# Kernel optimization log

Hardware: AMD Instinct MI355X
Metric: run time of the kernel (lower is better)

The kernel has to match this reference:

```python
import jax, jax.numpy as jnp
import numpy as np
import math

INPUT_SIZE = 128  # feature dim D, from init_kwargs

def setup_inputs() -> dict:
    key = jax.random.key(0)
    k1, k2 = jax.random.split(key)
    B, N, D = 4, 4096, INPUT_SIZE
    inp = jax.random.normal(k1, (B, N, D), dtype=jnp.float32)
    adj = jax.random.randint(k2, (B, N, N), 0, 2, dtype=jnp.int32)
    return {"input": inp, "adj": adj}

def reference(input, adj):
    # scores: [B, N, N] = X X^T / sqrt(D)
    scores = jnp.matmul(input, jnp.swapaxes(input, 1, 2)) / math.sqrt(INPUT_SIZE)
    neg = jnp.asarray(-1e12, dtype=scores.dtype)
    masked = jnp.where(adj > 0, scores, neg)
    attention = jax.nn.softmax(masked, axis=2)
    out_hid = jnp.matmul(attention, input)  # [B, N, D]
    return out_hid
```

## Files before the change

kernel.cpp:

```cpp
#include <hip/hip_runtime.h>
#include <hip/hip_bf16.h>


#define NN 4096
#define DD 128
#define BK 128
#define NT (NN / BK)

#define XBT_REL 32768
#define BUF1_OFF 65536
#define P_OFF 131072
#define P_WSTRIDE 2304
#define LDS_BYTES (P_OFF + 8 * P_WSTRIDE)

typedef __attribute__((ext_vector_type(8))) short bf16x8;
typedef __attribute__((ext_vector_type(16))) float f32x16;

static __device__ __forceinline__ unsigned f2bf(float f) {
    union { float f; unsigned u; } v; v.f = f;
    return (v.u + 0x7fffu + ((v.u >> 16) & 1u)) >> 16;
}

static __device__ __forceinline__ void gl_lds16(const void* g, void* l) {
    __builtin_amdgcn_global_load_lds(
        (const __attribute__((address_space(1))) unsigned*)g,
        (__attribute__((address_space(3))) unsigned*)l, 16, 0, 0);
}

__global__ __launch_bounds__(256)
void gat_prep(const float* __restrict__ X, unsigned short* __restrict__ xb,
              unsigned short* __restrict__ xbt) {
    __shared__ unsigned short tile[64][132];
    const int t = threadIdx.x;
    const int b  = blockIdx.x >> 6;
    const int kc = blockIdx.x & 63;
    const float* src = X + ((size_t)b * NN + kc * 64) * DD;
    unsigned short* xbo = xb + ((size_t)b * NN + kc * 64) * DD;

    #pragma unroll
    for (int it = 0; it < 8; ++it) {
        int f = it * 256 + t;
        int k = f >> 5, d4 = (f & 31) * 4;
        float4 v = *(const float4*)(src + (size_t)f * 4);
        uint2 pk;
        pk.x = f2bf(v.x) | (f2bf(v.y) << 16);
        pk.y = f2bf(v.z) | (f2bf(v.w) << 16);
        *(uint2*)(xbo + (size_t)f * 4) = pk;
        *(uint2*)(&tile[k][d4]) = pk;
    }
    __syncthreads();
    const int d = t >> 1, kb0 = (t & 1) * 32;
    unsigned short* dst = xbt + (size_t)b * DD * NN + (size_t)d * NN + kc * 64 + kb0;
    #pragma unroll
    for (int c = 0; c < 4; ++c) {
        union { uint4 o; unsigned short e[8]; } u;
        #pragma unroll
        for (int j = 0; j < 8; ++j) u.e[j] = tile[kb0 + c * 8 + j][d];
        *(uint4*)(dst + c * 8) = u.o;
    }
}

__global__ __launch_bounds__(512, 2)
void gat_fused(const unsigned short* __restrict__ xb,
               const unsigned short* __restrict__ xbt,
               const int* __restrict__ adj,
               float* __restrict__ out) {
    extern __shared__ char lds[];
    const int t = threadIdx.x;
    const int w = t >> 6, l = t & 63;
    const int l32 = l & 31, h5 = l >> 5;
    const int rw = w >> 2;
    const int kh = w & 3;
    const int bid  = blockIdx.x;
    const int b    = bid >> 6;
    const int row0 = (bid & 63) * 64;
    const int qbase = row0 + rw * 32;
    const int kbase = kh * 32;

    const char* xb_b  = (const char*)(xb  + (size_t)b * NN * DD);
    const char* xbt_b = (const char*)(xbt + (size_t)b * DD * NN);
    const int*  Ag    = adj + (size_t)b * NN * NN;
    float*      Og    = out + (size_t)b * NN * DD;

    bf16x8 qfrag[8];
    {
        const char* qp = xb_b + (size_t)(qbase + l32) * 256;
        #pragma unroll
        for (int c = 0; c < 8; ++c)
            qfrag[c] = *(const bf16x8*)(qp + c * 32 + h5 * 16);
    }

    int off_xb[4], off_xbt[4];
    #pragma unroll
    for (int j = 0; j < 4; ++j) {
        int r = w * 16 + 4 * j + (l >> 4);
        off_xb[j]  = r * 256      + (((l & 15) ^ (r & 7)) * 16);
        off_xbt[j] = r * (NN * 2) + (((l & 15) ^ (r & 7)) * 16);
    }
    char* bufA = lds;
    char* bufB = lds + BUF1_OFF;
    char* pw   = lds + P_OFF + w * P_WSTRIDE;
    const int* arow = Ag + (size_t)(qbase + l32) * NN + kbase + 4 * h5;

#define STAGE(BUF, KEY0) do {                                                  \
    _Pragma("unroll")                                                          \
    for (int j = 0; j < 4; ++j) {                                              \
        gl_lds16(xb_b  + (size_t)(KEY0) * 256 + off_xb[j],                     \
                 (BUF) + w * 4096 + j * 1024);                                 \
        gl_lds16(xbt_b + (size_t)(KEY0) * 2 + off_xbt[j],                      \
                 (BUF) + XBT_REL + w * 4096 + j * 1024);                       \
    }                                                                          \
} while (0)

    STAGE(bufA, 0);
    int4 avA[4];
    #pragma unroll
    for (int g = 0; g < 4; ++g) avA[g] = *(const int4*)(arow + g * 8);

    f32x16 oacc[4];
    #pragma unroll
    for (int d = 0; d < 4; ++d) oacc[d] = (f32x16)(0.0f);
    float psum = 0.f;

#define COMPUTE(BUF, AV) do {                                                  \
    f32x16 sacc = (f32x16)(0.0f);                                              \
    {                                                                          \
        const int krow = kbase + l32;                                          \
        const char* kp = (BUF) + krow * 256;                                   \
        const int sw = krow & 7;                                               \
        _Pragma("unroll")                                                      \
        for (int c = 0; c < 8; ++c) {                                          \
            bf16x8 kf = *(const bf16x8*)(kp + (((2 * c + h5) ^ sw) * 16));     \
            sacc = __builtin_amdgcn_mfma_f32_32x32x16_bf16(                    \
                kf, qfrag[c], sacc, 0, 0, 0);                                  \
        }                                                                      \
    }                                                                          \
    {                                                                          \
        const float SC = 0.08838834764831845f;                \
        _Pragma("unroll")                                                      \
        for (int g = 0; g < 4; ++g) {                                          \
            int4 a = (AV)[g];                                                  \
            float p0 = (a.x > 0) ? __expf(sacc[4 * g + 0] * SC) : 0.f;         \
            float p1 = (a.y > 0) ? __expf(sacc[4 * g + 1] * SC) : 0.f;         \
            float p2 = (a.z > 0) ? __expf(sacc[4 * g + 2] * SC) : 0.f;         \
            float p3 = (a.w > 0) ? __expf(sacc[4 * g + 3] * SC) : 0.f;         \
            psum += p0 + p1 + p2 + p3;                                         \
            uint2 pk;                                                          \
            pk.x = f2bf(p0) | (f2bf(p1) << 16);                                \
            pk.y = f2bf(p2) | (f2bf(p3) << 16);                                \
            *(uint2*)(pw + l32 * 72 + g * 16 + h5 * 8) = pk;                   \
        }                                                                      \
    }                                                                          \
    {                                                                          \
        bf16x8 pf0 = *(const bf16x8*)(pw + l32 * 72 + h5 * 16);                \
        bf16x8 pf1 = *(const bf16x8*)(pw + l32 * 72 + 32 + h5 * 16);           \
        _Pragma("unroll")                                                      \
        for (int db = 0; db < 4; ++db) {                                       \
            const int vrow = db * 32 + l32;                                    \
            const int swv = vrow & 7;                                          \
            const char* vp = (BUF) + XBT_REL + vrow * 256;                     \
            bf16x8 v0 = *(const bf16x8*)(vp + (((4 * kh + h5) ^ swv) * 16));   \
            oacc[db] = __builtin_amdgcn_mfma_f32_32x32x16_bf16(                \
                pf0, v0, oacc[db], 0, 0, 0);                                   \
            bf16x8 v1 = *(const bf16x8*)(vp + (((4 * kh + 2 + h5) ^ swv) * 16)); \
            oacc[db] = __builtin_amdgcn_mfma_f32_32x32x16_bf16(                \
                pf1, v1, oacc[db], 0, 0, 0);                                   \
        }                                                                      \
    }                                                                          \
} while (0)

    for (int kt = 0; kt < NT - 1; ++kt) {
        int4 avB[4];
        #pragma unroll
        for (int g = 0; g < 4; ++g)
            avB[g] = *(const int4*)(arow + (kt + 1) * BK + g * 8);
        asm volatile("s_waitcnt vmcnt(4)" ::: "memory");
        __builtin_amdgcn_s_barrier();
        STAGE(bufB, (kt + 1) * BK);
        COMPUTE(bufA, avA);
        char* tmp = bufA; bufA = bufB; bufB = tmp;
        #pragma unroll
        for (int g = 0; g < 4; ++g) avA[g] = avB[g];
    }
    asm volatile("s_waitcnt vmcnt(0)" ::: "memory");
    __builtin_amdgcn_s_barrier();
    COMPUTE(bufA, avA);

    psum += __shfl_xor(psum, 32, 64);
    __syncthreads();

    float* slot = (float*)(lds + w * 17408);
    #pragma unroll
    for (int db = 0; db < 4; ++db)
        #pragma unroll
        for (int r = 0; r < 16; ++r) {
            const int lrow = (r & 3) + 8 * (r >> 2) + 4 * h5;
            slot[lrow * 136 + db * 32 + l32] = oacc[db][r];
        }
    float* psarea = (float*)(lds + 139264);
    if (l < 32) psarea[w * 32 + l] = psum;
    __syncthreads();

    {
        const int R   = w * 8 + (l >> 3);
        const int q32 = R & 31, rwR = R >> 5;
        const int d0  = (l & 7) * 16;
        float tot = psarea[(rwR * 4 + 0) * 32 + q32]
                  + psarea[(rwR * 4 + 1) * 32 + q32]
                  + psarea[(rwR * 4 + 2) * 32 + q32]
                  + psarea[(rwR * 4 + 3) * 32 + q32];
        float invt = 1.0f / tot;
        float4 acc[4];
        #pragma unroll
        for (int j = 0; j < 4; ++j) acc[j] = (float4){0.f, 0.f, 0.f, 0.f};
        #pragma unroll
        for (int kx = 0; kx < 4; ++kx) {
            const float* sp = (const float*)(lds + (rwR * 4 + kx) * 17408)
                              + q32 * 136 + d0;
            #pragma unroll
            for (int j = 0; j < 4; ++j) {
                float4 v = *(const float4*)(sp + 4 * j);
                acc[j].x += v.x; acc[j].y += v.y;
                acc[j].z += v.z; acc[j].w += v.w;
            }
        }
        float* op = Og + (size_t)(row0 + R) * DD + d0;
        #pragma unroll
        for (int j = 0; j < 4; ++j) {
            float4 res;
            res.x = acc[j].x * invt; res.y = acc[j].y * invt;
            res.z = acc[j].z * invt; res.w = acc[j].w * invt;
            *(float4*)(op + 4 * j) = res;
        }
    }
#undef COMPUTE
#undef STAGE
}

extern "C" void kernel_launch(void* const* d_in, const int* in_sizes, int n_in,
                              void* d_out, int out_size, void* d_ws, size_t ws_size,
                              hipStream_t stream) {
    const float* X   = (const float*)d_in[0];
    const int*   adj = (const int*)d_in[1];
    float*       out = (float*)d_out;
    unsigned short* xb  = (unsigned short*)d_ws;
    unsigned short* xbt = xb + (size_t)4 * NN * DD;

    hipFuncSetAttribute((const void*)gat_fused,
                        hipFuncAttributeMaxDynamicSharedMemorySize, LDS_BYTES);
    gat_prep<<<dim3(256), dim3(256), 0, stream>>>(X, xb, xbt);
    gat_fused<<<dim3(256), dim3(512), LDS_BYTES, stream>>>(xb, xbt, adj, out);
}
```

Before: 415.4 us.

## Repack softmax probabilities in registers via permlane swap; prefetch adjacency two tiles ahead

Drops the per-wave LDS round trip that re-laid the bf16 probability tile from accumulator layout into MFMA A-operand layout. It now packs pairs with v_cvt_pk_bf16_f32 and exchanges halves across the wave with v_permlane32_swap. It also deepens the adjacency-mask prefetch from one tile ahead to two, hiding more global latency on the dominant int32 stream, and shrinks LDS use. The cost is more live registers, and the s_waitcnt vmcnt(4) count may no longer fit the extra in-flight loads, which could stall the loop or break its ordering.

```diff
diff --git a/kernel.cpp b/kernel.cpp
--- a/kernel.cpp
+++ b/kernel.cpp
@@ -9,9 +9,8 @@
 
 #define XBT_REL 32768
 #define BUF1_OFF 65536
-#define P_OFF 131072
-#define P_WSTRIDE 2304
-#define LDS_BYTES (P_OFF + 8 * P_WSTRIDE)
+#define PS_OFF 139264
+#define LDS_BYTES (PS_OFF + 1024)
 
 typedef __attribute__((ext_vector_type(8))) short bf16x8;
 typedef __attribute__((ext_vector_type(16))) float f32x16;
@@ -25,6 +24,15 @@
     __builtin_amdgcn_global_load_lds(
         (const __attribute__((address_space(1))) unsigned*)g,
         (__attribute__((address_space(3))) unsigned*)l, 16, 0, 0);
+}
+
+static __device__ __forceinline__ unsigned cvtpk(float lo, float hi) {
+    unsigned r;
+    asm("v_cvt_pk_bf16_f32 %0, %1, %2" : "=v"(r) : "v"(lo), "v"(hi));
+    return r;
+}
+static __device__ __forceinline__ void plswap(unsigned& a, unsigned& b) {
+    asm volatile("v_permlane32_swap_b32 %0, %1" : "+v"(a), "+v"(b));
 }
 
 __global__ __launch_bounds__(256)
@@ -99,7 +107,6 @@
     }
     char* bufA = lds;
     char* bufB = lds + BUF1_OFF;
-    char* pw   = lds + P_OFF + w * P_WSTRIDE;
     const int* arow = Ag + (size_t)(qbase + l32) * NN + kbase + 4 * h5;
 
 #define STAGE(BUF, KEY0) do {                                                  \
@@ -113,9 +120,11 @@
 } while (0)
 
     STAGE(bufA, 0);
-    int4 avA[4];
+    int4 avA[4], avB[4], avC[4];
     #pragma unroll
     for (int g = 0; g < 4; ++g) avA[g] = *(const int4*)(arow + g * 8);
+    #pragma unroll
+    for (int g = 0; g < 4; ++g) avB[g] = *(const int4*)(arow + BK + g * 8);
 
     f32x16 oacc[4];
     #pragma unroll
@@ -135,25 +144,33 @@
                 kf, qfrag[c], sacc, 0, 0, 0);                                  \
         }                                                                      \
     }                                                                          \
+    float p[16];                                                               \
     {                                                                          \
         const float SC = 0.08838834764831845f;                \
         _Pragma("unroll")                                                      \
         for (int g = 0; g < 4; ++g) {                                          \
             int4 a = (AV)[g];                                                  \
-            float p0 = (a.x > 0) ? __expf(sacc[4 * g + 0] * SC) : 0.f;         \
-            float p1 = (a.y > 0) ? __expf(sacc[4 * g + 1] * SC) : 0.f;         \
-            float p2 = (a.z > 0) ? __expf(sacc[4 * g + 2] * SC) : 0.f;         \
-            float p3 = (a.w > 0) ? __expf(sacc[4 * g + 3] * SC) : 0.f;         \
-            psum += p0 + p1 + p2 + p3;                                         \
-            uint2 pk;                                                          \
-            pk.x = f2bf(p0) | (f2bf(p1) << 16);                                \
-            pk.y = f2bf(p2) | (f2bf(p3) << 16);                                \
-            *(uint2*)(pw + l32 * 72 + g * 16 + h5 * 8) = pk;                   \
+            p[4*g+0] = (a.x > 0) ? __expf(sacc[4*g+0] * SC) : 0.f;             \
+            p[4*g+1] = (a.y > 0) ? __expf(sacc[4*g+1] * SC) : 0.f;             \
+            p[4*g+2] = (a.z > 0) ? __expf(sacc[4*g+2] * SC) : 0.f;             \
+            p[4*g+3] = (a.w > 0) ? __expf(sacc[4*g+3] * SC) : 0.f;             \
+            psum += p[4*g+0] + p[4*g+1] + p[4*g+2] + p[4*g+3];                 \
         }                                                                      \
     }                                                                          \
-    {                                                                          \
-        bf16x8 pf0 = *(const bf16x8*)(pw + l32 * 72 + h5 * 16);                \
-        bf16x8 pf1 = *(const bf16x8*)(pw + l32 * 72 + 32 + h5 * 16);           \
+      \
+      \
+    union { bf16x8 v; unsigned u[4]; } pf0u, pf1u;                             \
+    {                                                                          \
+        unsigned a0 = cvtpk(p[0],  p[1]),  b0 = cvtpk(p[4],  p[5]);            \
+        unsigned a1 = cvtpk(p[2],  p[3]),  b1 = cvtpk(p[6],  p[7]);            \
+        plswap(a0, b0);  plswap(a1, b1);                                       \
+        pf0u.u[0] = a0; pf0u.u[1] = a1; pf0u.u[2] = b0; pf0u.u[3] = b1;        \
+        unsigned a2 = cvtpk(p[8],  p[9]),  b2 = cvtpk(p[12], p[13]);           \
+        unsigned a3 = cvtpk(p[10], p[11]), b3 = cvtpk(p[14], p[15]);           \
+        plswap(a2, b2);  plswap(a3, b3);                                       \
+        pf1u.u[0] = a2; pf1u.u[1] = a3; pf1u.u[2] = b2; pf1u.u[3] = b3;        \
+    }                                                                          \
+    {                                                                          \
         _Pragma("unroll")                                                      \
         for (int db = 0; db < 4; ++db) {                                       \
             const int vrow = db * 32 + l32;                                    \
@@ -161,26 +178,27 @@
             const char* vp = (BUF) + XBT_REL + vrow * 256;                     \
             bf16x8 v0 = *(const bf16x8*)(vp + (((4 * kh + h5) ^ swv) * 16));   \
             oacc[db] = __builtin_amdgcn_mfma_f32_32x32x16_bf16(                \
-                pf0, v0, oacc[db], 0, 0, 0);                                   \
+                pf0u.v, v0, oacc[db], 0, 0, 0);                                \
             bf16x8 v1 = *(const bf16x8*)(vp + (((4 * kh + 2 + h5) ^ swv) * 16)); \
             oacc[db] = __builtin_amdgcn_mfma_f32_32x32x16_bf16(                \
-                pf1, v1, oacc[db], 0, 0, 0);                                   \
+                pf1u.v, v1, oacc[db], 0, 0, 0);                                \
         }                                                                      \
     }                                                                          \
 } while (0)
 
     for (int kt = 0; kt < NT - 1; ++kt) {
-        int4 avB[4];
-        #pragma unroll
-        for (int g = 0; g < 4; ++g)
-            avB[g] = *(const int4*)(arow + (kt + 1) * BK + g * 8);
         asm volatile("s_waitcnt vmcnt(4)" ::: "memory");
         __builtin_amdgcn_s_barrier();
         STAGE(bufB, (kt + 1) * BK);
+        if (kt + 2 < NT) {
+            #pragma unroll
+            for (int g = 0; g < 4; ++g)
+                avC[g] = *(const int4*)(arow + (kt + 2) * BK + g * 8);
+        }
         COMPUTE(bufA, avA);
         char* tmp = bufA; bufA = bufB; bufB = tmp;
         #pragma unroll
-        for (int g = 0; g < 4; ++g) avA[g] = avB[g];
+        for (int g = 0; g < 4; ++g) { avA[g] = avB[g]; avB[g] = avC[g]; }
     }
     asm volatile("s_waitcnt vmcnt(0)" ::: "memory");
     __builtin_amdgcn_s_barrier();
@@ -197,7 +215,7 @@
             const int lrow = (r & 3) + 8 * (r >> 2) + 4 * h5;
             slot[lrow * 136 + db * 32 + l32] = oacc[db][r];
         }
-    float* psarea = (float*)(lds + 139264);
+    float* psarea = (float*)(lds + PS_OFF);
     if (l < 32) psarea[w * 32 + l] = psum;
     __syncthreads();
 
```

Result: faster. 395.2 us (-4.9%).
